# Kernel optimization log

Measured on AMD Instinct MI355X. Metric: run time of the kernel, lower is better.

## Reference

```python
import jax, jax.numpy as jnp
import numpy as np

N_NODES = 50000
N_EDGES = 800000
IN_DIM = 128
HID_DIM = 64


def gcn_conv(x, W, b, src, dst, ew):
    """PyG GCNConv with edge_weight: add self-loops (weight 1), symmetric
    normalization D^-1/2 (A+I) D^-1/2, linear transform, scatter-add, bias."""
    n = x.shape[0]
    loop = jnp.arange(n)
    src_a = jnp.concatenate([src, loop])           # [E+N]
    dst_a = jnp.concatenate([dst, loop])
    ew_a = jnp.concatenate([ew, jnp.ones((n,), dtype=x.dtype)])
    deg = jax.ops.segment_sum(ew_a, dst_a, num_segments=n)   # [N]
    dinv = jnp.where(deg > 0, jax.lax.rsqrt(deg), 0.0)
    norm = dinv[src_a] * ew_a * dinv[dst_a]        # [E+N]
    h = x @ W                                      # [N, out]
    msg = h[src_a] * norm[:, None]                 # gather + scale
    out = jax.ops.segment_sum(msg, dst_a, num_segments=n)    # scatter-add
    return out + b


def setup_inputs() -> dict:
    key = jax.random.key(0)
    k = jax.random.split(key, 6)
    x = jax.random.normal(k[0], (N_NODES, IN_DIM), dtype=jnp.float32)
    edge_index = jax.random.randint(k[1], (2, N_EDGES), 0, N_NODES, dtype=jnp.int64)
    edge_weight = jax.random.uniform(k[2], (N_EDGES,), dtype=jnp.float32)
    W1 = jax.random.normal(k[3], (IN_DIM, HID_DIM), dtype=jnp.float32) * (1.0 / np.sqrt(IN_DIM))
    b1 = jnp.zeros((HID_DIM,), dtype=jnp.float32)
    W2 = jax.random.normal(k[4], (HID_DIM, 1), dtype=jnp.float32) * (1.0 / np.sqrt(HID_DIM))
    b2 = jnp.zeros((1,), dtype=jnp.float32)
    return {"x": x, "edge_index": edge_index, "edge_weight": edge_weight,
            "W1": W1, "b1": b1, "W2": W2, "b2": b2}


def reference(x, edge_index, edge_weight, W1, b1, W2, b2):
    src, dst = edge_index[0], edge_index[1]
    h = gcn_conv(x, W1, b1, src, dst, edge_weight)
    h = jax.nn.relu(h)
    h = gcn_conv(h, W2, b2, src, dst, edge_weight)
    return jax.nn.sigmoid(h).squeeze(-1)           # [N]
```

## Files before the change

kernel.cpp:

```cpp
#include <hip/hip_runtime.h>
#include <hip/hip_bf16.h>
#include <math.h>

#define N_NODES 50000
#define N_EDGES 800000
#define IN_DIM  128
#define HID_DIM 64

#define NBKT     196
#define BKT_CAP  5000
#define NPASSC   200
#define EDGES_PER_PASSC (N_EDGES / NPASSC)
#define GEMM_NODES 64
#define NGEMM    782
#define XS_LD    132

__global__ __launch_bounds__(256)
void partgemm_kernel(const int* __restrict__ src, const int* __restrict__ dst,
                     const float* __restrict__ ew,
                     int* __restrict__ cnt2d, int* __restrict__ off2d,
                     int2* __restrict__ edge_b,
                     const float* __restrict__ x, const float* __restrict__ W1,
                     __hip_bfloat16* __restrict__ h1b) {
    __shared__ float w1s[IN_DIM * HID_DIM];
    __shared__ float xs[GEMM_NODES][XS_LD];
    int bid = blockIdx.x;
    int tid = threadIdx.x;
    if (bid < NPASSC) {
        int* cnt1   = (int*)w1s;
        int* cnt2   = cnt1 + 256;
        int* runoff = cnt2 + 256;
        int* scuf   = runoff + 256;
        cnt1[tid] = 0; cnt2[tid] = 0;
        __syncthreads();
        int e0 = bid * EDGES_PER_PASSC;
        for (int i = tid; i < EDGES_PER_PASSC; i += 256)
            atomicAdd(&cnt1[dst[e0 + i] >> 8], 1);
        __syncthreads();
        scuf[tid] = cnt1[tid];
        __syncthreads();
#pragma unroll
        for (int off = 1; off < 256; off <<= 1) {
            int t = (tid >= off) ? scuf[tid - off] : 0;
            __syncthreads();
            scuf[tid] += t;
            __syncthreads();
        }
        int excl = scuf[tid] - cnt1[tid];
        if (tid < NBKT) {
            runoff[tid] = excl;
            cnt2d[bid * NBKT + tid] = cnt1[tid];
            off2d[bid * NBKT + tid] = excl;
        }
        __syncthreads();
        for (int i = tid; i < EDGES_PER_PASSC; i += 256) {
            int e = e0 + i;
            int d = dst[e];
            int b = d >> 8;
            int lr = atomicAdd(&cnt2[b], 1);
            int pos = bid * EDGES_PER_PASSC + runoff[b] + lr;
            edge_b[pos] = make_int2(src[e] | ((d & 255) << 16), __float_as_int(ew[e]));
        }
        return;
    }
    int gb = bid - NPASSC;
    int node0 = gb * GEMM_NODES;
    const float4* W4 = (const float4*)W1;
    float4* w1s4 = (float4*)w1s;
#pragma unroll
    for (int i = 0; i < 8; ++i) w1s4[tid + 256 * i] = W4[tid + 256 * i];
    {
        int r = tid >> 2, q = tid & 3;
        int row = node0 + r;
        if (row >= N_NODES) row = N_NODES - 1;
        const float4* xr = (const float4*)(x + (long)row * IN_DIM + q * 32);
#pragma unroll
        for (int i = 0; i < 8; ++i)
            *(float4*)&xs[r][q * 32 + i * 4] = xr[i];
    }
    __syncthreads();
    int w    = tid >> 6;
    int lane = tid & 63;
    int ng   = lane >> 2;
    int jg   = lane & 3;
    int j0   = w * 16 + jg * 4;
    float acc[4][4] = {{0.f}};
#pragma unroll 2
    for (int k = 0; k < IN_DIM; k += 4) {
        float4 wr0 = *(const float4*)&w1s[(k + 0) * HID_DIM + j0];
        float4 wr1 = *(const float4*)&w1s[(k + 1) * HID_DIM + j0];
        float4 wr2 = *(const float4*)&w1s[(k + 2) * HID_DIM + j0];
        float4 wr3 = *(const float4*)&w1s[(k + 3) * HID_DIM + j0];
#pragma unroll
        for (int i = 0; i < 4; ++i) {
            float4 xv = *(const float4*)&xs[ng + 16 * i][k];
            acc[i][0] += xv.x * wr0.x + xv.y * wr1.x + xv.z * wr2.x + xv.w * wr3.x;
            acc[i][1] += xv.x * wr0.y + xv.y * wr1.y + xv.z * wr2.y + xv.w * wr3.y;
            acc[i][2] += xv.x * wr0.z + xv.y * wr1.z + xv.z * wr2.z + xv.w * wr3.z;
            acc[i][3] += xv.x * wr0.w + xv.y * wr1.w + xv.z * wr2.w + xv.w * wr3.w;
        }
    }
#pragma unroll
    for (int i = 0; i < 4; ++i) {
        int n = node0 + ng + 16 * i;
        if (n < N_NODES) {
            __hip_bfloat16 bf[4];
            bf[0] = __float2bfloat16(acc[i][0]);
            bf[1] = __float2bfloat16(acc[i][1]);
            bf[2] = __float2bfloat16(acc[i][2]);
            bf[3] = __float2bfloat16(acc[i][3]);
            *(uint2*)&h1b[(long)n * HID_DIM + j0] = *(uint2*)bf;
        }
    }
}

__global__ __launch_bounds__(1024)
void bsort_kernel(const int* __restrict__ cnt2d, const int* __restrict__ off2d,
                  const int2* __restrict__ edge_b,
                  int2* __restrict__ edge_s, int* __restrict__ start_g,
                  int* __restrict__ cnt_g, float* __restrict__ dinv) {
    __shared__ int   cnt[256];
    __shared__ int   cnt2[256];
    __shared__ float deg[256];
    __shared__ int   sc[256];
    __shared__ int   fragbase[NPASSC + 1];
    __shared__ int   fragoff[NPASSC];
    int b   = blockIdx.x;
    int tid = threadIdx.x;
    int base = b * BKT_CAP;
    if (tid < 256) { cnt[tid] = 0; cnt2[tid] = 0; deg[tid] = 0.0f; }
    int fc = 0;
    if (tid < NPASSC) {
        fc = cnt2d[tid * NBKT + b];
        fragoff[tid] = off2d[tid * NBKT + b];
    }
    if (tid < 256) sc[tid] = fc;
    __syncthreads();
#pragma unroll
    for (int off = 1; off < 256; off <<= 1) {
        int t = (tid >= off && tid < 256) ? sc[tid - off] : 0;
        __syncthreads();
        if (tid < 256) sc[tid] += t;
        __syncthreads();
    }
    if (tid < NPASSC) fragbase[tid] = sc[tid] - fc;
    if (tid == NPASSC - 1) fragbase[NPASSC] = sc[tid];
    __syncthreads();
    int M = fragbase[NPASSC];
    for (int i = tid; i < M; i += 1024) {
        int lo = 0, hi = NPASSC - 1;
        while (lo < hi) { int mid = (lo + hi + 1) >> 1; if (fragbase[mid] <= i) lo = mid; else hi = mid - 1; }
        int2 e = edge_b[lo * EDGES_PER_PASSC + fragoff[lo] + (i - fragbase[lo])];
        int ld = (e.x >> 16) & 255;
        atomicAdd(&cnt[ld], 1);
        atomicAdd(&deg[ld], __int_as_float(e.y));
    }
    __syncthreads();
    if (tid < 256) sc[tid] = cnt[tid];
    __syncthreads();
#pragma unroll
    for (int off = 1; off < 256; off <<= 1) {
        int t = (tid >= off && tid < 256) ? sc[tid - off] : 0;
        __syncthreads();
        if (tid < 256) sc[tid] += t;
        __syncthreads();
    }
    if (tid < 256) {
        int startL = sc[tid] - cnt[tid];
        int node = b * 256 + tid;
        if (node < N_NODES) {
            start_g[node] = base + startL;
            cnt_g[node]   = cnt[tid];
            dinv[node]    = rsqrtf(1.0f + deg[tid]);
        }
        sc[tid] = startL;
    }
    __syncthreads();
    for (int i = tid; i < M; i += 1024) {
        int lo = 0, hi = NPASSC - 1;
        while (lo < hi) { int mid = (lo + hi + 1) >> 1; if (fragbase[mid] <= i) lo = mid; else hi = mid - 1; }
        int2 e = edge_b[lo * EDGES_PER_PASSC + fragoff[lo] + (i - fragbase[lo])];
        int ld = (e.x >> 16) & 255;
        int r = atomicAdd(&cnt2[ld], 1);
        edge_s[base + sc[ld] + r] = make_int2(e.x & 0xFFFF, e.y);
    }
}

__global__ void gather1_layer2_kernel(const int* __restrict__ start_g, const int* __restrict__ cnt_g,
                                      const int2* __restrict__ edge_s,
                                      const __hip_bfloat16* __restrict__ h1b,
                                      const float* __restrict__ dinv, const float* __restrict__ b1,
                                      const float* __restrict__ W2, float* __restrict__ h2s) {
    __shared__ int2 meta[4][64];
    int wave = (blockIdx.x * blockDim.x + threadIdx.x) >> 6;
    int wl = threadIdx.x >> 6;
    int lane = threadIdx.x & 63;
    if (wave >= N_NODES) return;
    int s0 = start_g[wave];
    int ctotal = cnt_g[wave];
    int c0 = (lane & 31) * 2;
    int half = lane >> 5;
    float accA = 0.f, accB = 0.f, accA2 = 0.f, accB2 = 0.f;
    for (int done = 0; done < ctotal; done += 64) {
        int cnt = ctotal - done;
        if (cnt > 64) cnt = 64;
        if (lane < cnt) {
            int2 m = edge_s[s0 + done + lane];
            float w = __int_as_float(m.y) * dinv[m.x];
            meta[wl][lane] = make_int2(m.x, __float_as_int(w));
        }
        __builtin_amdgcn_wave_barrier();
        int cnte = cnt & ~1;
        int j = 0;
        for (; j + 16 <= cnte; j += 16) {
            int2 m0 = meta[wl][j +  0 + half];
            int2 m1 = meta[wl][j +  2 + half];
            int2 m2 = meta[wl][j +  4 + half];
            int2 m3 = meta[wl][j +  6 + half];
            int2 m4 = meta[wl][j +  8 + half];
            int2 m5 = meta[wl][j + 10 + half];
            int2 m6 = meta[wl][j + 12 + half];
            int2 m7 = meta[wl][j + 14 + half];
            unsigned int p0 = *(const unsigned int*)&h1b[m0.x * HID_DIM + c0];
            unsigned int p1 = *(const unsigned int*)&h1b[m1.x * HID_DIM + c0];
            unsigned int p2 = *(const unsigned int*)&h1b[m2.x * HID_DIM + c0];
            unsigned int p3 = *(const unsigned int*)&h1b[m3.x * HID_DIM + c0];
            unsigned int p4 = *(const unsigned int*)&h1b[m4.x * HID_DIM + c0];
            unsigned int p5 = *(const unsigned int*)&h1b[m5.x * HID_DIM + c0];
            unsigned int p6 = *(const unsigned int*)&h1b[m6.x * HID_DIM + c0];
            unsigned int p7 = *(const unsigned int*)&h1b[m7.x * HID_DIM + c0];
            float w0 = __int_as_float(m0.y), w1 = __int_as_float(m1.y);
            float w2 = __int_as_float(m2.y), w3 = __int_as_float(m3.y);
            float w4 = __int_as_float(m4.y), w5 = __int_as_float(m5.y);
            float w6 = __int_as_float(m6.y), w7 = __int_as_float(m7.y);
            accA  += w0 * __uint_as_float(p0 << 16);
            accB  += w0 * __uint_as_float(p0 & 0xFFFF0000u);
            accA2 += w1 * __uint_as_float(p1 << 16);
            accB2 += w1 * __uint_as_float(p1 & 0xFFFF0000u);
            accA  += w2 * __uint_as_float(p2 << 16);
            accB  += w2 * __uint_as_float(p2 & 0xFFFF0000u);
            accA2 += w3 * __uint_as_float(p3 << 16);
            accB2 += w3 * __uint_as_float(p3 & 0xFFFF0000u);
            accA  += w4 * __uint_as_float(p4 << 16);
            accB  += w4 * __uint_as_float(p4 & 0xFFFF0000u);
            accA2 += w5 * __uint_as_float(p5 << 16);
            accB2 += w5 * __uint_as_float(p5 & 0xFFFF0000u);
            accA  += w6 * __uint_as_float(p6 << 16);
            accB  += w6 * __uint_as_float(p6 & 0xFFFF0000u);
            accA2 += w7 * __uint_as_float(p7 << 16);
            accB2 += w7 * __uint_as_float(p7 & 0xFFFF0000u);
        }
        for (; j + 2 <= cnte; j += 2) {
            int2 m = meta[wl][j + half];
            unsigned int p = *(const unsigned int*)&h1b[m.x * HID_DIM + c0];
            accA += __int_as_float(m.y) * __uint_as_float(p << 16);
            accB += __int_as_float(m.y) * __uint_as_float(p & 0xFFFF0000u);
        }
        if ((cnt & 1) && half == 0) {
            int2 m = meta[wl][cnt - 1];
            unsigned int p = *(const unsigned int*)&h1b[m.x * HID_DIM + c0];
            accA += __int_as_float(m.y) * __uint_as_float(p << 16);
            accB += __int_as_float(m.y) * __uint_as_float(p & 0xFFFF0000u);
        }
        __builtin_amdgcn_wave_barrier();
    }
    accA += accA2; accB += accB2;
    accA += __shfl_xor(accA, 32, 64);
    accB += __shfl_xor(accB, 32, 64);
    float di = dinv[wave];
    unsigned int sp = *(const unsigned int*)&h1b[wave * HID_DIM + c0];
    float s0f = __uint_as_float(sp << 16);
    float s1f = __uint_as_float(sp & 0xFFFF0000u);
    float z0 = di * (accA + di * s0f) + b1[c0];
    float z1 = di * (accB + di * s1f) + b1[c0 + 1];
    float h0  = fmaxf(z0, 0.0f);
    float h1v = fmaxf(z1, 0.0f);
    float v = h0 * W2[c0] + h1v * W2[c0 + 1];
#pragma unroll
    for (int off = 16; off > 0; off >>= 1)
        v += __shfl_down(v, off, 32);
    if (lane == 0) h2s[wave] = v * di;
}

__global__ void gather2_final_kernel(const int* __restrict__ start_g, const int* __restrict__ cnt_g,
                                     const int2* __restrict__ edge_s,
                                     const float* __restrict__ h2s, const float* __restrict__ dinv,
                                     const float* __restrict__ b2, float* __restrict__ out) {
    int t = blockIdx.x * blockDim.x + threadIdx.x;
    int n = t >> 4;
    int sub = t & 15;
    if (n >= N_NODES) return;
    int s0 = start_g[n];
    int cnt = cnt_g[n];
    float acc = 0.0f;
    for (int j = sub; j < cnt; j += 16) {
        int2 m = edge_s[s0 + j];
        acc += __int_as_float(m.y) * h2s[m.x];
    }
#pragma unroll
    for (int off = 8; off > 0; off >>= 1)
        acc += __shfl_down(acc, off, 16);
    if (sub == 0) {
        float z = dinv[n] * (acc + h2s[n]) + b2[0];
        out[n] = 1.0f / (1.0f + expf(-z));
    }
}

extern "C" void kernel_launch(void* const* d_in, const int* in_sizes, int n_in,
                              void* d_out, int out_size, void* d_ws, size_t ws_size,
                              hipStream_t stream) {
    const float* x  = (const float*)d_in[0];
    const int*   ei = (const int*)d_in[1];
    const float* ew = (const float*)d_in[2];
    const float* W1 = (const float*)d_in[3];
    const float* b1 = (const float*)d_in[4];
    const float* W2 = (const float*)d_in[5];
    const float* b2 = (const float*)d_in[6];
    float* out = (float*)d_out;

    const int* src = ei;
    const int* dst = ei + N_EDGES;

    char* ws = (char*)d_ws;
    int2*  edge_b  = (int2*)ws;              ws += (size_t)N_EDGES * sizeof(int2);
    int2*  edge_s  = (int2*)ws;              ws += (size_t)NBKT * BKT_CAP * sizeof(int2);
    int*   cnt2d   = (int*)ws;               ws += (size_t)NPASSC * NBKT * sizeof(int);
    int*   off2d   = (int*)ws;               ws += (size_t)NPASSC * NBKT * sizeof(int);
    int*   start_g = (int*)ws;               ws += N_NODES * sizeof(int);
    int*   cnt_g   = (int*)ws;               ws += N_NODES * sizeof(int);
    float* dinv    = (float*)ws;             ws += N_NODES * sizeof(float);
    float* h2s     = (float*)ws;             ws += N_NODES * sizeof(float);
    ws = (char*)(((uintptr_t)ws + 127) & ~(uintptr_t)127);
    __hip_bfloat16* h1b = (__hip_bfloat16*)ws;

    partgemm_kernel<<<NPASSC + NGEMM, 256, 0, stream>>>(src, dst, ew, cnt2d, off2d, edge_b, x, W1, h1b);
    bsort_kernel<<<NBKT, 1024, 0, stream>>>(cnt2d, off2d, edge_b, edge_s, start_g, cnt_g, dinv);
    gather1_layer2_kernel<<<(N_NODES * 64) / 256, 256, 0, stream>>>(start_g, cnt_g, edge_s, h1b, dinv, b1, W2, h2s);
    gather2_final_kernel<<<(N_NODES * 16 + 255) / 256, 256, 0, stream>>>(start_g, cnt_g, edge_s, h2s, dinv, b2, out);
}
```

Measured before the change: 158.4 us.

## Replace per-node CSR sort with per-bucket LDS atomic scatter aggregation

Removes the full in-bucket counting sort (edge_s, start_g, cnt_g) and instead aggregates messages directly from the partitioned edge buckets. Each 256-node bucket block accumulates its 64-wide layer-1 features in a 64KB shared-memory tile using LDS float atomics, then applies bias, ReLU and W2 in the same kernel. Degree and layer-2 are likewise done with shared atomics per bucket. This drops a sort pass and its global writes, but it launches only 196 blocks for the heavy gather, and each wave processes edges serially with one 2-byte load per lane per edge, which risks poor parallelism and latency-bound gathers.

```diff
diff --git a/kernel.cpp b/kernel.cpp
--- a/kernel.cpp
+++ b/kernel.cpp
@@ -8,7 +8,6 @@
 #define HID_DIM 64
 
 #define NBKT     196
-#define BKT_CAP  5000
 #define NPASSC   200
 #define EDGES_PER_PASSC (N_EDGES / NPASSC)
 #define GEMM_NODES 64
@@ -114,195 +113,117 @@
     }
 }
 
-__global__ __launch_bounds__(1024)
-void bsort_kernel(const int* __restrict__ cnt2d, const int* __restrict__ off2d,
-                  const int2* __restrict__ edge_b,
-                  int2* __restrict__ edge_s, int* __restrict__ start_g,
-                  int* __restrict__ cnt_g, float* __restrict__ dinv) {
-    __shared__ int   cnt[256];
-    __shared__ int   cnt2[256];
-    __shared__ float deg[256];
-    __shared__ int   sc[256];
-    __shared__ int   fragbase[NPASSC + 1];
-    __shared__ int   fragoff[NPASSC];
+__global__ __launch_bounds__(256)
+void deg_kernel(const int* __restrict__ cnt2d, const int* __restrict__ off2d,
+                const int2* __restrict__ edge_b, float* __restrict__ dinv) {
+    __shared__ float degs[256];
+    __shared__ int   cntS[NPASSC];
+    __shared__ int   offS[NPASSC];
     int b   = blockIdx.x;
     int tid = threadIdx.x;
-    int base = b * BKT_CAP;
-    if (tid < 256) { cnt[tid] = 0; cnt2[tid] = 0; deg[tid] = 0.0f; }
-    int fc = 0;
+    int wv   = tid >> 6;
+    int lane = tid & 63;
+    degs[tid] = 0.0f;
     if (tid < NPASSC) {
-        fc = cnt2d[tid * NBKT + b];
-        fragoff[tid] = off2d[tid * NBKT + b];
-    }
-    if (tid < 256) sc[tid] = fc;
-    __syncthreads();
-#pragma unroll
-    for (int off = 1; off < 256; off <<= 1) {
-        int t = (tid >= off && tid < 256) ? sc[tid - off] : 0;
-        __syncthreads();
-        if (tid < 256) sc[tid] += t;
-        __syncthreads();
-    }
-    if (tid < NPASSC) fragbase[tid] = sc[tid] - fc;
-    if (tid == NPASSC - 1) fragbase[NPASSC] = sc[tid];
-    __syncthreads();
-    int M = fragbase[NPASSC];
-    for (int i = tid; i < M; i += 1024) {
-        int lo = 0, hi = NPASSC - 1;
-        while (lo < hi) { int mid = (lo + hi + 1) >> 1; if (fragbase[mid] <= i) lo = mid; else hi = mid - 1; }
-        int2 e = edge_b[lo * EDGES_PER_PASSC + fragoff[lo] + (i - fragbase[lo])];
-        int ld = (e.x >> 16) & 255;
-        atomicAdd(&cnt[ld], 1);
-        atomicAdd(&deg[ld], __int_as_float(e.y));
-    }
-    __syncthreads();
-    if (tid < 256) sc[tid] = cnt[tid];
-    __syncthreads();
-#pragma unroll
-    for (int off = 1; off < 256; off <<= 1) {
-        int t = (tid >= off && tid < 256) ? sc[tid - off] : 0;
-        __syncthreads();
-        if (tid < 256) sc[tid] += t;
-        __syncthreads();
-    }
-    if (tid < 256) {
-        int startL = sc[tid] - cnt[tid];
-        int node = b * 256 + tid;
-        if (node < N_NODES) {
-            start_g[node] = base + startL;
-            cnt_g[node]   = cnt[tid];
-            dinv[node]    = rsqrtf(1.0f + deg[tid]);
-        }
-        sc[tid] = startL;
-    }
-    __syncthreads();
-    for (int i = tid; i < M; i += 1024) {
-        int lo = 0, hi = NPASSC - 1;
-        while (lo < hi) { int mid = (lo + hi + 1) >> 1; if (fragbase[mid] <= i) lo = mid; else hi = mid - 1; }
-        int2 e = edge_b[lo * EDGES_PER_PASSC + fragoff[lo] + (i - fragbase[lo])];
-        int ld = (e.x >> 16) & 255;
-        int r = atomicAdd(&cnt2[ld], 1);
-        edge_s[base + sc[ld] + r] = make_int2(e.x & 0xFFFF, e.y);
-    }
-}
-
-__global__ void gather1_layer2_kernel(const int* __restrict__ start_g, const int* __restrict__ cnt_g,
-                                      const int2* __restrict__ edge_s,
-                                      const __hip_bfloat16* __restrict__ h1b,
-                                      const float* __restrict__ dinv, const float* __restrict__ b1,
-                                      const float* __restrict__ W2, float* __restrict__ h2s) {
-    __shared__ int2 meta[4][64];
-    int wave = (blockIdx.x * blockDim.x + threadIdx.x) >> 6;
-    int wl = threadIdx.x >> 6;
-    int lane = threadIdx.x & 63;
-    if (wave >= N_NODES) return;
-    int s0 = start_g[wave];
-    int ctotal = cnt_g[wave];
-    int c0 = (lane & 31) * 2;
-    int half = lane >> 5;
-    float accA = 0.f, accB = 0.f, accA2 = 0.f, accB2 = 0.f;
-    for (int done = 0; done < ctotal; done += 64) {
-        int cnt = ctotal - done;
-        if (cnt > 64) cnt = 64;
-        if (lane < cnt) {
-            int2 m = edge_s[s0 + done + lane];
-            float w = __int_as_float(m.y) * dinv[m.x];
-            meta[wl][lane] = make_int2(m.x, __float_as_int(w));
-        }
-        __builtin_amdgcn_wave_barrier();
-        int cnte = cnt & ~1;
-        int j = 0;
-        for (; j + 16 <= cnte; j += 16) {
-            int2 m0 = meta[wl][j +  0 + half];
-            int2 m1 = meta[wl][j +  2 + half];
-            int2 m2 = meta[wl][j +  4 + half];
-            int2 m3 = meta[wl][j +  6 + half];
-            int2 m4 = meta[wl][j +  8 + half];
-            int2 m5 = meta[wl][j + 10 + half];
-            int2 m6 = meta[wl][j + 12 + half];
-            int2 m7 = meta[wl][j + 14 + half];
-            unsigned int p0 = *(const unsigned int*)&h1b[m0.x * HID_DIM + c0];
-            unsigned int p1 = *(const unsigned int*)&h1b[m1.x * HID_DIM + c0];
-            unsigned int p2 = *(const unsigned int*)&h1b[m2.x * HID_DIM + c0];
-            unsigned int p3 = *(const unsigned int*)&h1b[m3.x * HID_DIM + c0];
-            unsigned int p4 = *(const unsigned int*)&h1b[m4.x * HID_DIM + c0];
-            unsigned int p5 = *(const unsigned int*)&h1b[m5.x * HID_DIM + c0];
-            unsigned int p6 = *(const unsigned int*)&h1b[m6.x * HID_DIM + c0];
-            unsigned int p7 = *(const unsigned int*)&h1b[m7.x * HID_DIM + c0];
-            float w0 = __int_as_float(m0.y), w1 = __int_as_float(m1.y);
-            float w2 = __int_as_float(m2.y), w3 = __int_as_float(m3.y);
-            float w4 = __int_as_float(m4.y), w5 = __int_as_float(m5.y);
-            float w6 = __int_as_float(m6.y), w7 = __int_as_float(m7.y);
-            accA  += w0 * __uint_as_float(p0 << 16);
-            accB  += w0 * __uint_as_float(p0 & 0xFFFF0000u);
-            accA2 += w1 * __uint_as_float(p1 << 16);
-            accB2 += w1 * __uint_as_float(p1 & 0xFFFF0000u);
-            accA  += w2 * __uint_as_float(p2 << 16);
-            accB  += w2 * __uint_as_float(p2 & 0xFFFF0000u);
-            accA2 += w3 * __uint_as_float(p3 << 16);
-            accB2 += w3 * __uint_as_float(p3 & 0xFFFF0000u);
-            accA  += w4 * __uint_as_float(p4 << 16);
-            accB  += w4 * __uint_as_float(p4 & 0xFFFF0000u);
-            accA2 += w5 * __uint_as_float(p5 << 16);
-            accB2 += w5 * __uint_as_float(p5 & 0xFFFF0000u);
-            accA  += w6 * __uint_as_float(p6 << 16);
-            accB  += w6 * __uint_as_float(p6 & 0xFFFF0000u);
-            accA2 += w7 * __uint_as_float(p7 << 16);
-            accB2 += w7 * __uint_as_float(p7 & 0xFFFF0000u);
-        }
-        for (; j + 2 <= cnte; j += 2) {
-            int2 m = meta[wl][j + half];
-            unsigned int p = *(const unsigned int*)&h1b[m.x * HID_DIM + c0];
-            accA += __int_as_float(m.y) * __uint_as_float(p << 16);
-            accB += __int_as_float(m.y) * __uint_as_float(p & 0xFFFF0000u);
-        }
-        if ((cnt & 1) && half == 0) {
-            int2 m = meta[wl][cnt - 1];
-            unsigned int p = *(const unsigned int*)&h1b[m.x * HID_DIM + c0];
-            accA += __int_as_float(m.y) * __uint_as_float(p << 16);
-            accB += __int_as_float(m.y) * __uint_as_float(p & 0xFFFF0000u);
-        }
-        __builtin_amdgcn_wave_barrier();
-    }
-    accA += accA2; accB += accB2;
-    accA += __shfl_xor(accA, 32, 64);
-    accB += __shfl_xor(accB, 32, 64);
-    float di = dinv[wave];
-    unsigned int sp = *(const unsigned int*)&h1b[wave * HID_DIM + c0];
-    float s0f = __uint_as_float(sp << 16);
-    float s1f = __uint_as_float(sp & 0xFFFF0000u);
-    float z0 = di * (accA + di * s0f) + b1[c0];
-    float z1 = di * (accB + di * s1f) + b1[c0 + 1];
-    float h0  = fmaxf(z0, 0.0f);
-    float h1v = fmaxf(z1, 0.0f);
-    float v = h0 * W2[c0] + h1v * W2[c0 + 1];
-#pragma unroll
-    for (int off = 16; off > 0; off >>= 1)
-        v += __shfl_down(v, off, 32);
-    if (lane == 0) h2s[wave] = v * di;
-}
-
-__global__ void gather2_final_kernel(const int* __restrict__ start_g, const int* __restrict__ cnt_g,
-                                     const int2* __restrict__ edge_s,
-                                     const float* __restrict__ h2s, const float* __restrict__ dinv,
-                                     const float* __restrict__ b2, float* __restrict__ out) {
-    int t = blockIdx.x * blockDim.x + threadIdx.x;
-    int n = t >> 4;
-    int sub = t & 15;
-    if (n >= N_NODES) return;
-    int s0 = start_g[n];
-    int cnt = cnt_g[n];
-    float acc = 0.0f;
-    for (int j = sub; j < cnt; j += 16) {
-        int2 m = edge_s[s0 + j];
-        acc += __int_as_float(m.y) * h2s[m.x];
-    }
-#pragma unroll
-    for (int off = 8; off > 0; off >>= 1)
-        acc += __shfl_down(acc, off, 16);
-    if (sub == 0) {
-        float z = dinv[n] * (acc + h2s[n]) + b2[0];
-        out[n] = 1.0f / (1.0f + expf(-z));
+        cntS[tid] = cnt2d[tid * NBKT + b];
+        offS[tid] = off2d[tid * NBKT + b];
+    }
+    __syncthreads();
+    for (int f = wv; f < NPASSC; f += 4) {
+        int mf = cntS[f];
+        long fb = (long)f * EDGES_PER_PASSC + offS[f];
+        for (int j = lane; j < mf; j += 64) {
+            int2 e = edge_b[fb + j];
+            atomicAdd(&degs[(e.x >> 16) & 255], __int_as_float(e.y));
+        }
+    }
+    __syncthreads();
+    int node = b * 256 + tid;
+    if (node < N_NODES) dinv[node] = rsqrtf(1.0f + degs[tid]);
+}
+
+__global__ __launch_bounds__(1024)
+void bgather1_kernel(const int* __restrict__ cnt2d, const int* __restrict__ off2d,
+                     const int2* __restrict__ edge_b,
+                     const __hip_bfloat16* __restrict__ h1b,
+                     const float* __restrict__ dinv, const float* __restrict__ b1,
+                     const float* __restrict__ W2, float* __restrict__ h2s) {
+    __shared__ float acc[256][HID_DIM];
+    __shared__ int   cntS[NPASSC];
+    __shared__ int   offS[NPASSC];
+    int b    = blockIdx.x;
+    int tid  = threadIdx.x;
+    int wv   = tid >> 6;
+    int lane = tid & 63;
+    if (tid < NPASSC) {
+        cntS[tid] = cnt2d[tid * NBKT + b];
+        offS[tid] = off2d[tid * NBKT + b];
+    }
+    float4* accv = (float4*)&acc[0][0];
+#pragma unroll
+    for (int i = 0; i < 4; ++i) accv[tid + 1024 * i] = make_float4(0.f, 0.f, 0.f, 0.f);
+    __syncthreads();
+    const unsigned short* h1u = (const unsigned short*)h1b;
+    for (int f = wv; f < NPASSC; f += 16) {
+        int mf = cntS[f];
+        long fb = (long)f * EDGES_PER_PASSC + offS[f];
+        for (int j = 0; j < mf; ++j) {
+            int2 e = edge_b[fb + j];
+            int ld = (e.x >> 16) & 255;
+            int s  = e.x & 0xFFFF;
+            float wdi = __int_as_float(e.y) * dinv[s];
+            unsigned short us = h1u[(long)s * HID_DIM + lane];
+            atomicAdd(&acc[ld][lane], wdi * __uint_as_float((unsigned)us << 16));
+        }
+    }
+    __syncthreads();
+    for (int ln = wv; ln < 256; ln += 16) {
+        int node = b * 256 + ln;
+        if (node >= N_NODES) break;
+        float di = dinv[node];
+        float self = __uint_as_float((unsigned)h1u[(long)node * HID_DIM + lane] << 16);
+        float z = di * (acc[ln][lane] + di * self) + b1[lane];
+        float h = fmaxf(z, 0.0f);
+        float v = h * W2[lane];
+#pragma unroll
+        for (int off = 32; off > 0; off >>= 1)
+            v += __shfl_down(v, off, 64);
+        if (lane == 0) h2s[node] = v * di;
+    }
+}
+
+__global__ __launch_bounds__(256)
+void bgather2_kernel(const int* __restrict__ cnt2d, const int* __restrict__ off2d,
+                     const int2* __restrict__ edge_b,
+                     const float* __restrict__ h2s, const float* __restrict__ dinv,
+                     const float* __restrict__ b2, float* __restrict__ out) {
+    __shared__ float acc2[256];
+    __shared__ int   cntS[NPASSC];
+    __shared__ int   offS[NPASSC];
+    int b    = blockIdx.x;
+    int tid  = threadIdx.x;
+    int wv   = tid >> 6;
+    int lane = tid & 63;
+    acc2[tid] = 0.0f;
+    if (tid < NPASSC) {
+        cntS[tid] = cnt2d[tid * NBKT + b];
+        offS[tid] = off2d[tid * NBKT + b];
+    }
+    __syncthreads();
+    for (int f = wv; f < NPASSC; f += 4) {
+        int mf = cntS[f];
+        long fb = (long)f * EDGES_PER_PASSC + offS[f];
+        for (int j = lane; j < mf; j += 64) {
+            int2 e = edge_b[fb + j];
+            atomicAdd(&acc2[(e.x >> 16) & 255],
+                      __int_as_float(e.y) * h2s[e.x & 0xFFFF]);
+        }
+    }
+    __syncthreads();
+    int node = b * 256 + tid;
+    if (node < N_NODES) {
+        float z = dinv[node] * (acc2[tid] + h2s[node]) + b2[0];
+        out[node] = 1.0f / (1.0f + expf(-z));
     }
 }
 
@@ -323,18 +244,15 @@
 
     char* ws = (char*)d_ws;
     int2*  edge_b  = (int2*)ws;              ws += (size_t)N_EDGES * sizeof(int2);
-    int2*  edge_s  = (int2*)ws;              ws += (size_t)NBKT * BKT_CAP * sizeof(int2);
     int*   cnt2d   = (int*)ws;               ws += (size_t)NPASSC * NBKT * sizeof(int);
     int*   off2d   = (int*)ws;               ws += (size_t)NPASSC * NBKT * sizeof(int);
-    int*   start_g = (int*)ws;               ws += N_NODES * sizeof(int);
-    int*   cnt_g   = (int*)ws;               ws += N_NODES * sizeof(int);
     float* dinv    = (float*)ws;             ws += N_NODES * sizeof(float);
     float* h2s     = (float*)ws;             ws += N_NODES * sizeof(float);
     ws = (char*)(((uintptr_t)ws + 127) & ~(uintptr_t)127);
     __hip_bfloat16* h1b = (__hip_bfloat16*)ws;
 
     partgemm_kernel<<<NPASSC + NGEMM, 256, 0, stream>>>(src, dst, ew, cnt2d, off2d, edge_b, x, W1, h1b);
-    bsort_kernel<<<NBKT, 1024, 0, stream>>>(cnt2d, off2d, edge_b, edge_s, start_g, cnt_g, dinv);
-    gather1_layer2_kernel<<<(N_NODES * 64) / 256, 256, 0, stream>>>(start_g, cnt_g, edge_s, h1b, dinv, b1, W2, h2s);
-    gather2_final_kernel<<<(N_NODES * 16 + 255) / 256, 256, 0, stream>>>(start_g, cnt_g, edge_s, h2s, dinv, b2, out);
-}
+    deg_kernel<<<NBKT, 256, 0, stream>>>(cnt2d, off2d, edge_b, dinv);
+    bgather1_kernel<<<NBKT, 1024, 0, stream>>>(cnt2d, off2d, edge_b, h1b, dinv, b1, W2, h2s);
+    bgather2_kernel<<<NBKT, 256, 0, stream>>>(cnt2d, off2d, edge_b, h2s, dinv, b2, out);
+}
```

New measurement: 518.2 us. 227% more time.

## Stage edge chunks in LDS and stage bucket fragments in shared memory

Applied to the files above, without the earlier changes.

The partition phase now splits edges into 800 blocks of 1000. Each block reads src/dst/ew once, packs the edges into LDS and scatters them from LDS, where before it re-read global memory in a second pass. The bucket-sort kernel now copies each pass's fragment into a shared-memory buffer, one thread per fragment, using a 1024-wide scan. Both later passes then read from LDS, which removes the per-edge binary search and the repeated global reads. The cost is more passes (a larger cnt2d/off2d), serial per-thread fragment copies, and a 40KB LDS buffer that can overflow if a bucket holds more than BKT_CAP edges.

```diff
diff --git a/kernel.cpp b/kernel.cpp
--- a/kernel.cpp
+++ b/kernel.cpp
@@ -9,8 +9,8 @@
 
 #define NBKT     196
 #define BKT_CAP  5000
-#define NPASSC   200
-#define EDGES_PER_PASSC (N_EDGES / NPASSC)
+#define NPASSC   800
+#define EPB      1000
 #define GEMM_NODES 64
 #define NGEMM    782
 #define XS_LD    132
@@ -27,15 +27,26 @@
     int bid = blockIdx.x;
     int tid = threadIdx.x;
     if (bid < NPASSC) {
-        int* cnt1   = (int*)w1s;
+        int2*           epack = (int2*)w1s;
+        unsigned short* ebkt  = (unsigned short*)(epack + EPB);
+        int* cnt1   = (int*)xs;
         int* cnt2   = cnt1 + 256;
         int* runoff = cnt2 + 256;
         int* scuf   = runoff + 256;
         cnt1[tid] = 0; cnt2[tid] = 0;
         __syncthreads();
-        int e0 = bid * EDGES_PER_PASSC;
-        for (int i = tid; i < EDGES_PER_PASSC; i += 256)
-            atomicAdd(&cnt1[dst[e0 + i] >> 8], 1);
+        int e0 = bid * EPB;
+#pragma unroll
+        for (int it = 0; it < 4; ++it) {
+            int i = tid + 256 * it;
+            if (i < EPB) {
+                int e = e0 + i;
+                int d = dst[e];
+                epack[i] = make_int2(src[e] | ((d & 255) << 16), __float_as_int(ew[e]));
+                ebkt[i]  = (unsigned short)(d >> 8);
+                atomicAdd(&cnt1[d >> 8], 1);
+            }
+        }
         __syncthreads();
         scuf[tid] = cnt1[tid];
         __syncthreads();
@@ -53,13 +64,14 @@
             off2d[bid * NBKT + tid] = excl;
         }
         __syncthreads();
-        for (int i = tid; i < EDGES_PER_PASSC; i += 256) {
-            int e = e0 + i;
-            int d = dst[e];
-            int b = d >> 8;
-            int lr = atomicAdd(&cnt2[b], 1);
-            int pos = bid * EDGES_PER_PASSC + runoff[b] + lr;
-            edge_b[pos] = make_int2(src[e] | ((d & 255) << 16), __float_as_int(ew[e]));
+#pragma unroll
+        for (int it = 0; it < 4; ++it) {
+            int i = tid + 256 * it;
+            if (i < EPB) {
+                int b = ebkt[i];
+                int lr = atomicAdd(&cnt2[b], 1);
+                edge_b[bid * EPB + runoff[b] + lr] = epack[i];
+            }
         }
         return;
     }
@@ -119,38 +131,43 @@
                   const int2* __restrict__ edge_b,
                   int2* __restrict__ edge_s, int* __restrict__ start_g,
                   int* __restrict__ cnt_g, float* __restrict__ dinv) {
+    __shared__ int2  ebuf[BKT_CAP];
     __shared__ int   cnt[256];
     __shared__ int   cnt2[256];
     __shared__ float deg[256];
     __shared__ int   sc[256];
+    __shared__ int   fs[1024];
     __shared__ int   fragbase[NPASSC + 1];
-    __shared__ int   fragoff[NPASSC];
     int b   = blockIdx.x;
     int tid = threadIdx.x;
     int base = b * BKT_CAP;
     if (tid < 256) { cnt[tid] = 0; cnt2[tid] = 0; deg[tid] = 0.0f; }
-    int fc = 0;
+    int fc = 0, foff = 0;
     if (tid < NPASSC) {
-        fc = cnt2d[tid * NBKT + b];
-        fragoff[tid] = off2d[tid * NBKT + b];
-    }
-    if (tid < 256) sc[tid] = fc;
-    __syncthreads();
-#pragma unroll
-    for (int off = 1; off < 256; off <<= 1) {
-        int t = (tid >= off && tid < 256) ? sc[tid - off] : 0;
-        __syncthreads();
-        if (tid < 256) sc[tid] += t;
-        __syncthreads();
-    }
-    if (tid < NPASSC) fragbase[tid] = sc[tid] - fc;
-    if (tid == NPASSC - 1) fragbase[NPASSC] = sc[tid];
+        fc   = cnt2d[tid * NBKT + b];
+        foff = off2d[tid * NBKT + b];
+    }
+    fs[tid] = fc;
+    __syncthreads();
+#pragma unroll
+    for (int off = 1; off < 1024; off <<= 1) {
+        int t = (tid >= off) ? fs[tid - off] : 0;
+        __syncthreads();
+        fs[tid] += t;
+        __syncthreads();
+    }
+    if (tid < NPASSC) fragbase[tid] = fs[tid] - fc;
+    if (tid == 0) fragbase[NPASSC] = fs[1023];
     __syncthreads();
     int M = fragbase[NPASSC];
+    if (tid < NPASSC) {
+        int fb = fragbase[tid];
+        const int2* srcp = edge_b + (long)tid * EPB + foff;
+        for (int j = 0; j < fc; ++j) ebuf[fb + j] = srcp[j];
+    }
+    __syncthreads();
     for (int i = tid; i < M; i += 1024) {
-        int lo = 0, hi = NPASSC - 1;
-        while (lo < hi) { int mid = (lo + hi + 1) >> 1; if (fragbase[mid] <= i) lo = mid; else hi = mid - 1; }
-        int2 e = edge_b[lo * EDGES_PER_PASSC + fragoff[lo] + (i - fragbase[lo])];
+        int2 e = ebuf[i];
         int ld = (e.x >> 16) & 255;
         atomicAdd(&cnt[ld], 1);
         atomicAdd(&deg[ld], __int_as_float(e.y));
@@ -177,9 +194,7 @@
     }
     __syncthreads();
     for (int i = tid; i < M; i += 1024) {
-        int lo = 0, hi = NPASSC - 1;
-        while (lo < hi) { int mid = (lo + hi + 1) >> 1; if (fragbase[mid] <= i) lo = mid; else hi = mid - 1; }
-        int2 e = edge_b[lo * EDGES_PER_PASSC + fragoff[lo] + (i - fragbase[lo])];
+        int2 e = ebuf[i];
         int ld = (e.x >> 16) & 255;
         int r = atomicAdd(&cnt2[ld], 1);
         edge_s[base + sc[ld] + r] = make_int2(e.x & 0xFFFF, e.y);
@@ -322,7 +337,7 @@
     const int* dst = ei + N_EDGES;
 
     char* ws = (char*)d_ws;
-    int2*  edge_b  = (int2*)ws;              ws += (size_t)N_EDGES * sizeof(int2);
+    int2*  edge_b  = (int2*)ws;              ws += (size_t)NPASSC * EPB * sizeof(int2);
     int2*  edge_s  = (int2*)ws;              ws += (size_t)NBKT * BKT_CAP * sizeof(int2);
     int*   cnt2d   = (int*)ws;               ws += (size_t)NPASSC * NBKT * sizeof(int);
     int*   off2d   = (int*)ws;               ws += (size_t)NPASSC * NBKT * sizeof(int);
```

New measurement: 161.8 us. +2.2%, slower.
